# Optimization experiments

Hardware: AMD Instinct MI355X
Metric: run time of the kernel (lower is better)

The kernel has to match this reference:

```python
import jax, jax.numpy as jnp
import numpy as np

EPS = 1e-5
NEG_INF = float('-inf')

B, L, D = 4, 1024, 1024
H = 16
HD = D // H
I = 3280  # _round_to_multiple(3.2 * 1024, 8)
WIN = 256
STD = 0.01


def rmsnorm(x, w):
    x = jnp.clip(x.astype(jnp.float32), -10000.0, 10000.0)
    rms = jnp.sqrt(jnp.maximum(jnp.mean(x * x, axis=-1, keepdims=True), EPS) + EPS)
    out = x / rms * w
    return jnp.where(jnp.isfinite(out), out, jnp.zeros_like(out))


def setup_inputs() -> dict:
    key = jax.random.key(0)
    ks = jax.random.split(key, 12)
    inp = {
        'x': jax.random.normal(ks[0], (B, L, D), dtype=jnp.float32),
        'wq_w': jax.random.normal(ks[1], (D, D), dtype=jnp.float32) * STD,
        'wq_b': jnp.zeros((D,), jnp.float32),
        'wk_w': jax.random.normal(ks[2], (D, D), dtype=jnp.float32) * STD,
        'wk_b': jnp.zeros((D,), jnp.float32),
        'wv_w': jax.random.normal(ks[3], (D, D), dtype=jnp.float32) * STD,
        'wv_b': jnp.zeros((D,), jnp.float32),
        'wo_w': jax.random.normal(ks[4], (D, D), dtype=jnp.float32) * STD,
        'wo_b': jnp.zeros((D,), jnp.float32),
        'q_norm_w': jnp.ones((HD,), jnp.float32),
        'k_norm_w': jnp.ones((HD,), jnp.float32),
        'seq_norm_w': jnp.ones((D,), jnp.float32),
        'seq_post_norm_w': jnp.ones((D,), jnp.float32),
        'ffn_norm_w': jnp.ones((D,), jnp.float32),
        'ffn_post_norm_w': jnp.ones((D,), jnp.float32),
        'w1_w': jax.random.normal(ks[5], (I, D), dtype=jnp.float32) * STD,
        'w1_b': jnp.zeros((I,), jnp.float32),
        'w2_w': jax.random.normal(ks[6], (D, I), dtype=jnp.float32) * STD,
        'w2_b': jnp.zeros((D,), jnp.float32),
        'w3_w': jax.random.normal(ks[7], (I, D), dtype=jnp.float32) * STD,
        'w3_b': jnp.zeros((I,), jnp.float32),
        'window_size': WIN,
    }
    return inp


def attention(x, wq_w, wq_b, wk_w, wk_b, wv_w, wv_b, wo_w, wo_b, q_norm_w, k_norm_w, window_size):
    b, l, d = x.shape
    x = x.astype(jnp.float32)
    q = (x @ wq_w.T + wq_b).reshape(b, l, H, HD)
    k = (x @ wk_w.T + wk_b).reshape(b, l, H, HD)
    v = (x @ wv_w.T + wv_b).reshape(b, l, H, HD)
    q = rmsnorm(q, q_norm_w)
    k = rmsnorm(k, k_norm_w)
    scale = HD ** -0.5
    scores = jnp.einsum('blhd,bmhd->bhlm', q, k) * scale
    i = jnp.arange(l)[:, None]
    j = jnp.arange(l)[None, :]
    masked = (j > i) | (i - j >= window_size)  # True => forbidden
    scores = scores + jnp.where(masked, NEG_INF, 0.0)
    p = jax.nn.softmax(scores, axis=-1)
    attn = jnp.einsum('bhlm,bmhd->blhd', p, v)
    attn = jnp.where(jnp.isfinite(attn), attn, jnp.zeros_like(attn))
    attn = attn.reshape(b, l, d)
    return attn @ wo_w.T + wo_b


def swiglu(x, w1_w, w1_b, w2_w, w2_b, w3_w, w3_b):
    x = x.astype(jnp.float32)
    z1 = x @ w1_w.T + w1_b
    z3 = x @ w3_w.T + w3_b
    return (jax.nn.silu(z1) * z3) @ w2_w.T + w2_b


def reference(x, wq_w, wq_b, wk_w, wk_b, wv_w, wv_b, wo_w, wo_b,
              q_norm_w, k_norm_w, seq_norm_w, seq_post_norm_w,
              ffn_norm_w, ffn_post_norm_w,
              w1_w, w1_b, w2_w, w2_b, w3_w, w3_b, window_size):
    # seq_norm -> attn -> seq_post_norm -> residual
    a = attention(rmsnorm(x, seq_norm_w), wq_w, wq_b, wk_w, wk_b, wv_w, wv_b,
                  wo_w, wo_b, q_norm_w, k_norm_w, window_size)
    h = x + rmsnorm(a, seq_post_norm_w)
    # ffn_norm -> ffn -> ffn_post_norm -> residual
    f = swiglu(rmsnorm(h, ffn_norm_w), w1_w, w1_b, w2_w, w2_b, w3_w, w3_b)
    return h + rmsnorm(f, ffn_post_norm_w)
```

## Files before the change

kernel.cpp:

```cpp
#include <hip/hip_runtime.h>
#include <cmath>
#include <cstdint>

typedef __bf16 bf16;
typedef bf16 bf16x4 __attribute__((ext_vector_type(4)));
typedef bf16 bf16x8 __attribute__((ext_vector_type(8)));
typedef float f32x4 __attribute__((ext_vector_type(4)));
typedef unsigned int u32;
typedef u32 u32x4 __attribute__((ext_vector_type(4)));

#define EPS 1e-5f

__device__ __forceinline__ float clipf(float v) {
    return fminf(fmaxf(v, -10000.0f), 10000.0f);
}
__device__ __forceinline__ float fin0(float v) { return isfinite(v) ? v : 0.0f; }

__device__ __forceinline__ void async_copy16(void* lds, const void* g) {
    __builtin_amdgcn_global_load_lds((__attribute__((address_space(1))) void*)(void*)g,
                                     (__attribute__((address_space(3))) void*)lds,
                                     16, 0, 0);
}

__global__ __launch_bounds__(256) void prep(const float* __restrict__ wq, const float* __restrict__ wk,
                                            const float* __restrict__ wv, const float* __restrict__ wo,
                                            bf16* __restrict__ Wq, bf16* __restrict__ Wk,
                                            bf16* __restrict__ Wv, bf16* __restrict__ Wo,
                                            const float* __restrict__ w1, const float* __restrict__ w3,
                                            bf16* __restrict__ W1p, bf16* __restrict__ W3p,
                                            const float* __restrict__ w2, bf16* __restrict__ W2p,
                                            const float* __restrict__ x, const float* __restrict__ snw,
                                            bf16* __restrict__ xn) {
    const int bid = blockIdx.x, t = threadIdx.x;
    if (bid < 4096) {
        int z = bid >> 10, r = bid & 1023;
        const float* in = (z == 0) ? wq : (z == 1) ? wk : (z == 2) ? wv : wo;
        bf16* out = (z == 0) ? Wq : (z == 1) ? Wk : (z == 2) ? Wv : Wo;
        f32x4 v = ((const f32x4*)(in + (size_t)r * 1024))[t];
        bf16x4 o = {(bf16)v[0], (bf16)v[1], (bf16)v[2], (bf16)v[3]};
        ((bf16x4*)(out + (size_t)r * 1024))[t] = o;
    } else if (bid < 10752) {
        int b2 = bid - 4096;
        int which = b2 >= 3328;
        int r = b2 - (which ? 3328 : 0);
        const float* in = which ? w3 : w1;
        bf16* out = which ? W3p : W1p;
        bf16x4 o = {(bf16)0.f, (bf16)0.f, (bf16)0.f, (bf16)0.f};
        if (r < 3280) {
            f32x4 v = ((const f32x4*)(in + (size_t)r * 1024))[t];
            o[0] = (bf16)v[0]; o[1] = (bf16)v[1]; o[2] = (bf16)v[2]; o[3] = (bf16)v[3];
        }
        ((bf16x4*)(out + (size_t)r * 1024))[t] = o;
    } else if (bid < 11776) {
        int r = bid - 10752;
        for (int c4 = t * 4; c4 < 3328; c4 += 1024) {
            bf16x4 o = {(bf16)0.f, (bf16)0.f, (bf16)0.f, (bf16)0.f};
            if (c4 + 3 < 3280) {
                f32x4 v = *(const f32x4*)(w2 + (size_t)r * 3280 + c4);
                o[0] = (bf16)v[0]; o[1] = (bf16)v[1]; o[2] = (bf16)v[2]; o[3] = (bf16)v[3];
            } else {
                #pragma unroll
                for (int j = 0; j < 4; ++j)
                    if (c4 + j < 3280) o[j] = (bf16)w2[(size_t)r * 3280 + c4 + j];
            }
            *(bf16x4*)(W2p + (size_t)r * 3328 + c4) = o;
        }
    } else {
        __shared__ float sred[4];
        int row = bid - 11776;
        f32x4 xv = ((const f32x4*)(x + (size_t)row * 1024))[t];
        f32x4 cv;
        cv[0] = clipf(xv[0]); cv[1] = clipf(xv[1]); cv[2] = clipf(xv[2]); cv[3] = clipf(xv[3]);
        float ss = cv[0]*cv[0] + cv[1]*cv[1] + cv[2]*cv[2] + cv[3]*cv[3];
        #pragma unroll
        for (int off = 32; off >= 1; off >>= 1) ss += __shfl_xor(ss, off, 64);
        if ((t & 63) == 0) sred[t >> 6] = ss;
        __syncthreads();
        float tot = sred[0] + sred[1] + sred[2] + sred[3];
        float rms = sqrtf(fmaxf(tot * (1.0f / 1024.0f), EPS) + EPS);
        f32x4 wv_ = ((const f32x4*)snw)[t];
        bf16x4 o;
        o[0] = (bf16)fin0(cv[0] / rms * wv_[0]);
        o[1] = (bf16)fin0(cv[1] / rms * wv_[1]);
        o[2] = (bf16)fin0(cv[2] / rms * wv_[2]);
        o[3] = (bf16)fin0(cv[3] / rms * wv_[3]);
        *(bf16x4*)(xn + (size_t)row * 1024 + t * 4) = o;
    }
}

__global__ __launch_bounds__(512) void gemm_qkv3(const bf16* __restrict__ A,
                                                 const bf16* __restrict__ Bq,
                                                 const bf16* __restrict__ Bk,
                                                 const bf16* __restrict__ Bv,
                                                 const float* __restrict__ biq,
                                                 const float* __restrict__ bik,
                                                 const float* __restrict__ biv,
                                                 const float* __restrict__ qnw,
                                                 const float* __restrict__ knw,
                                                 bf16* __restrict__ Cq,
                                                 bf16* __restrict__ Ck,
                                                 bf16* __restrict__ VT) {
    __shared__ __align__(16) bf16 sA[2][128 * 32];
    __shared__ __align__(16) bf16 sBq[2][128 * 32];
    __shared__ __align__(16) bf16 sBk[2][128 * 32];
    __shared__ __align__(16) bf16 sBv[2][128 * 32];
    const int tid = threadIdx.x;
    const int w = tid >> 6, lane = tid & 63;
    const int m0 = blockIdx.x * 128;
    const int n0 = blockIdx.y * 128;
    const int mwo = (w >> 1) * 32;
    const int nwo = (w & 1) * 64;
    const int r16 = lane & 15, quad = lane >> 4;
    const int kreg = quad * 8;
    const int K = 1024, N = 1024;

    f32x4 zero = {0.f, 0.f, 0.f, 0.f};
    f32x4 aq[2][4], ak[2][4], av[2][4];
    #pragma unroll
    for (int i = 0; i < 2; ++i)
        #pragma unroll
        for (int j = 0; j < 4; ++j) { aq[i][j] = zero; ak[i][j] = zero; av[i][j] = zero; }

    const int arow = tid >> 2, akoff = (tid & 3) << 3;

    {
        async_copy16(&sA[0][tid * 8],  &A[(size_t)(m0 + arow) * K + akoff]);
        async_copy16(&sBq[0][tid * 8], &Bq[(size_t)(n0 + arow) * K + akoff]);
        async_copy16(&sBk[0][tid * 8], &Bk[(size_t)(n0 + arow) * K + akoff]);
        async_copy16(&sBv[0][tid * 8], &Bv[(size_t)(n0 + arow) * K + akoff]);
    }
    for (int kt = 0; kt < 32; ++kt) {
        __syncthreads();
        const int cur = kt & 1, nxt = cur ^ 1;
        if (kt + 1 < 32) {
            const int kb = (kt + 1) << 5;
            async_copy16(&sA[nxt][tid * 8],  &A[(size_t)(m0 + arow) * K + kb + akoff]);
            async_copy16(&sBq[nxt][tid * 8], &Bq[(size_t)(n0 + arow) * K + kb + akoff]);
            async_copy16(&sBk[nxt][tid * 8], &Bk[(size_t)(n0 + arow) * K + kb + akoff]);
            async_copy16(&sBv[nxt][tid * 8], &Bv[(size_t)(n0 + arow) * K + kb + akoff]);
        }
        bf16x8 af[2], bq_[4], bk_[4], bv_[4];
        #pragma unroll
        for (int i = 0; i < 2; ++i)
            af[i] = *(const bf16x8*)&sA[cur][(mwo + i * 16 + r16) * 32 + kreg];
        #pragma unroll
        for (int i = 0; i < 4; ++i) {
            bq_[i] = *(const bf16x8*)&sBq[cur][(nwo + i * 16 + r16) * 32 + kreg];
            bk_[i] = *(const bf16x8*)&sBk[cur][(nwo + i * 16 + r16) * 32 + kreg];
            bv_[i] = *(const bf16x8*)&sBv[cur][(nwo + i * 16 + r16) * 32 + kreg];
        }
        #pragma unroll
        for (int mi = 0; mi < 2; ++mi)
            #pragma unroll
            for (int ni = 0; ni < 4; ++ni) {
                aq[mi][ni] = __builtin_amdgcn_mfma_f32_16x16x32_bf16(af[mi], bq_[ni], aq[mi][ni], 0, 0, 0);
                ak[mi][ni] = __builtin_amdgcn_mfma_f32_16x16x32_bf16(af[mi], bk_[ni], ak[mi][ni], 0, 0, 0);
                av[mi][ni] = __builtin_amdgcn_mfma_f32_16x16x32_bf16(af[mi], bv_[ni], av[mi][ni], 0, 0, 0);
            }
    }

    float nwq[4], nwk[4], bvq[4], bvk[4], bvv[4];
    #pragma unroll
    for (int ni = 0; ni < 4; ++ni) {
        int col = n0 + nwo + ni * 16 + r16;
        bvq[ni] = biq[col]; bvk[ni] = bik[col]; bvv[ni] = biv[col];
        nwq[ni] = qnw[ni * 16 + r16]; nwk[ni] = knw[ni * 16 + r16];
    }
    #pragma unroll
    for (int s = 0; s < 2; ++s) {
        bf16* C = s ? Ck : Cq;
        #pragma unroll
        for (int mi = 0; mi < 2; ++mi) {
            #pragma unroll
            for (int r = 0; r < 4; ++r) {
                float v[4], ss = 0.0f;
                #pragma unroll
                for (int ni = 0; ni < 4; ++ni) {
                    float a = s ? ak[mi][ni][r] : aq[mi][ni][r];
                    v[ni] = clipf(a + (s ? bvk[ni] : bvq[ni]));
                    ss += v[ni] * v[ni];
                }
                ss += __shfl_xor(ss, 1, 64);
                ss += __shfl_xor(ss, 2, 64);
                ss += __shfl_xor(ss, 4, 64);
                ss += __shfl_xor(ss, 8, 64);
                float rms = sqrtf(fmaxf(ss * (1.0f / 64.0f), EPS) + EPS);
                int row = m0 + mwo + mi * 16 + quad * 4 + r;
                #pragma unroll
                for (int ni = 0; ni < 4; ++ni) {
                    int col = n0 + nwo + ni * 16 + r16;
                    float nw = s ? nwk[ni] : nwq[ni];
                    C[(size_t)row * N + col] = (bf16)fin0(v[ni] / rms * nw);
                }
            }
        }
    }
    {
        const int b_ = m0 >> 10;
        const int tokbase = (m0 & 1023) + mwo;
        #pragma unroll
        for (int ni = 0; ni < 4; ++ni) {
            int col = n0 + nwo + ni * 16 + r16;
            int h_ = col >> 6, hd = col & 63;
            bf16* dst = VT + (((size_t)b_ * 16 + h_) * 64 + hd) * 1024;
            #pragma unroll
            for (int mi = 0; mi < 2; ++mi) {
                bf16x4 pack;
                #pragma unroll
                for (int r = 0; r < 4; ++r) pack[r] = (bf16)(av[mi][ni][r] + bvv[ni]);
                *(bf16x4*)&dst[tokbase + mi * 16 + quad * 4] = pack;
            }
        }
    }
}

__global__ __launch_bounds__(512) void attn_win(const bf16* __restrict__ q,
                                                const bf16* __restrict__ k,
                                                const bf16* __restrict__ vt,
                                                const int* __restrict__ winp,
                                                bf16* __restrict__ o) {
    __shared__ __align__(16) bf16 sQ[128 * 64];
    __shared__ __align__(16) bf16 sK[64 * 64];
    __shared__ __align__(16) bf16 sVt[64 * 80];
    __shared__ __align__(16) bf16 sP[128 * 64];
    const int tid = threadIdx.x, w = tid >> 6, lane = tid & 63;
    const int qt = blockIdx.x, h = blockIdx.y, b = blockIdx.z;
    const int q0 = qt * 128;
    const int win = *winp;
    const float scale = 0.125f;
    const int r16 = lane & 15, quad = lane >> 4;

    {
        int c0 = tid, c1 = tid + 512;
        async_copy16(&sQ[c0 * 8], &q[(((size_t)b * 1024 + q0 + (c0 >> 3)) * 16 + h) * 64 + (c0 & 7) * 8]);
        async_copy16(&sQ[c1 * 8], &q[(((size_t)b * 1024 + q0 + (c1 >> 3)) * 16 + h) * 64 + (c1 & 7) * 8]);
    }
    __syncthreads();
    bf16x8 aq0 = *(const bf16x8*)&sQ[(w * 16 + r16) * 64 + quad * 8];
    bf16x8 aq1 = *(const bf16x8*)&sQ[(w * 16 + r16) * 64 + 32 + quad * 8];

    float Lr[4];
    f32x4 zero = {0.f, 0.f, 0.f, 0.f};
    f32x4 accO[4];
    #pragma unroll
    for (int r = 0; r < 4; ++r) Lr[r] = 0.0f;
    #pragma unroll
    for (int nf = 0; nf < 4; ++nf) accO[nf] = zero;

    int lo = q0 - (win - 1); if (lo < 0) lo = 0;
    const int kt0 = lo >> 6;
    const int ktend = (q0 + 127) >> 6;
    const bf16* vth = vt + ((size_t)b * 16 + h) * 64 * 1024;

    for (int kt = kt0; kt <= ktend; ++kt) {
        __syncthreads();
        async_copy16(&sK[tid * 8], &k[(((size_t)b * 1024 + kt * 64 + (tid >> 3)) * 16 + h) * 64 + (tid & 7) * 8]);
        {
            int hd = tid >> 3, koff = (tid & 7) * 8;
            *(u32x4*)&sVt[hd * 80 + koff] = *(const u32x4*)&vth[(size_t)hd * 1024 + kt * 64 + koff];
        }
        __syncthreads();

        f32x4 sf[4];
        #pragma unroll
        for (int nf = 0; nf < 4; ++nf) {
            bf16x8 bk0 = *(const bf16x8*)&sK[(nf * 16 + r16) * 64 + quad * 8];
            bf16x8 bk1 = *(const bf16x8*)&sK[(nf * 16 + r16) * 64 + 32 + quad * 8];
            f32x4 accS = zero;
            accS = __builtin_amdgcn_mfma_f32_16x16x32_bf16(aq0, bk0, accS, 0, 0, 0);
            accS = __builtin_amdgcn_mfma_f32_16x16x32_bf16(aq1, bk1, accS, 0, 0, 0);
            sf[nf] = accS;
        }

        #pragma unroll
        for (int r = 0; r < 4; ++r) {
            int i = q0 + w * 16 + quad * 4 + r;
            float ps = 0.0f;
            #pragma unroll
            for (int nf = 0; nf < 4; ++nf) {
                int j = kt * 64 + nf * 16 + r16;
                bool ok = (j <= i) && (i - j < win);
                float pv = ok ? __expf(sf[nf][r] * scale - 8.0f) : 0.0f;
                ps += pv;
                sP[(w * 16 + quad * 4 + r) * 64 + nf * 16 + r16] = (bf16)pv;
            }
            Lr[r] += ps;
        }
        __syncthreads();

        bf16x8 ap0 = *(const bf16x8*)&sP[(w * 16 + r16) * 64 + quad * 8];
        bf16x8 ap1 = *(const bf16x8*)&sP[(w * 16 + r16) * 64 + 32 + quad * 8];
        #pragma unroll
        for (int nf = 0; nf < 4; ++nf) {
            bf16x8 bv0 = *(const bf16x8*)&sVt[(nf * 16 + r16) * 80 + quad * 8];
            bf16x8 bv1 = *(const bf16x8*)&sVt[(nf * 16 + r16) * 80 + 32 + quad * 8];
            accO[nf] = __builtin_amdgcn_mfma_f32_16x16x32_bf16(ap0, bv0, accO[nf], 0, 0, 0);
            accO[nf] = __builtin_amdgcn_mfma_f32_16x16x32_bf16(ap1, bv1, accO[nf], 0, 0, 0);
        }
    }

    #pragma unroll
    for (int r = 0; r < 4; ++r) {
        float l = Lr[r];
        l += __shfl_xor(l, 1, 64);
        l += __shfl_xor(l, 2, 64);
        l += __shfl_xor(l, 4, 64);
        l += __shfl_xor(l, 8, 64);
        float inv = (l > 0.0f) ? 1.0f / l : 0.0f;
        int row = q0 + w * 16 + quad * 4 + r;
        #pragma unroll
        for (int nf = 0; nf < 4; ++nf) {
            float ov = fin0(accO[nf][r] * inv);
            o[(((size_t)b * 1024 + row) * 16 + h) * 64 + nf * 16 + r16] = (bf16)ov;
        }
    }
}

__global__ __launch_bounds__(512) void gemm_sk2(const bf16* __restrict__ A,
                                                const bf16* __restrict__ B,
                                                float* __restrict__ P,
                                                int K, int Kh) {
    __shared__ __align__(16) bf16 sA[2][256 * 32];
    __shared__ __align__(16) bf16 sB[2][128 * 32];
    const int tid = threadIdx.x;
    const int w = tid >> 6, lane = tid & 63;
    const int m0 = blockIdx.x * 256, n0 = blockIdx.y * 128;
    const int mwo = (w & 3) * 64, nwo = (w >> 2) * 64;
    const int r16 = lane & 15, quad = lane >> 4, kreg = quad * 8;
    const int kbase = blockIdx.z * Kh;
    const int N = 1024;

    const int ar0 = tid >> 2,        ak0 = (tid & 3) << 3;
    const int c1 = tid + 512;
    const int ar1 = c1 >> 2,         ak1 = (c1 & 3) << 3;
    const int br = tid >> 2,         bk = (tid & 3) << 3;

    f32x4 zero = {0.f, 0.f, 0.f, 0.f};
    f32x4 acc[4][4];
    #pragma unroll
    for (int i = 0; i < 4; ++i)
        #pragma unroll
        for (int j = 0; j < 4; ++j) acc[i][j] = zero;

    {
        async_copy16(&sA[0][tid * 8], &A[(size_t)(m0 + ar0) * K + kbase + ak0]);
        async_copy16(&sA[0][c1 * 8],  &A[(size_t)(m0 + ar1) * K + kbase + ak1]);
        async_copy16(&sB[0][tid * 8], &B[(size_t)(n0 + br) * K + kbase + bk]);
    }
    const int kIters = Kh >> 5;
    for (int kt = 0; kt < kIters; ++kt) {
        __syncthreads();
        const int cur = kt & 1, nxt = cur ^ 1;
        if (kt + 1 < kIters) {
            const int kb = kbase + ((kt + 1) << 5);
            async_copy16(&sA[nxt][tid * 8], &A[(size_t)(m0 + ar0) * K + kb + ak0]);
            async_copy16(&sA[nxt][c1 * 8],  &A[(size_t)(m0 + ar1) * K + kb + ak1]);
            async_copy16(&sB[nxt][tid * 8], &B[(size_t)(n0 + br) * K + kb + bk]);
        }
        bf16x8 af[4], bfr[4];
        #pragma unroll
        for (int i = 0; i < 4; ++i) {
            af[i]  = *(const bf16x8*)&sA[cur][(mwo + i * 16 + r16) * 32 + kreg];
            bfr[i] = *(const bf16x8*)&sB[cur][(nwo + i * 16 + r16) * 32 + kreg];
        }
        #pragma unroll
        for (int mi = 0; mi < 4; ++mi)
            #pragma unroll
            for (int ni = 0; ni < 4; ++ni)
                acc[mi][ni] = __builtin_amdgcn_mfma_f32_16x16x32_bf16(af[mi], bfr[ni], acc[mi][ni], 0, 0, 0);
    }

    float* Pz = P + (size_t)blockIdx.z * 4096 * 1024;
    #pragma unroll
    for (int mi = 0; mi < 4; ++mi)
        #pragma unroll
        for (int ni = 0; ni < 4; ++ni) {
            int col = n0 + nwo + ni * 16 + r16;
            #pragma unroll
            for (int r = 0; r < 4; ++r) {
                int row = m0 + mwo + mi * 16 + quad * 4 + r;
                Pz[(size_t)row * N + col] = acc[mi][ni][r];
            }
        }
}

template <bool EMIT>
__global__ __launch_bounds__(512) void resid_norm(const float* __restrict__ xres,
                                                  const float* __restrict__ p0,
                                                  const float* __restrict__ p1,
                                                  const float* __restrict__ bias,
                                                  const float* __restrict__ wpost,
                                                  const float* __restrict__ wnext,
                                                  float* __restrict__ hout,
                                                  bf16* __restrict__ hnout) {
    __shared__ float sred[8];
    const int tid = threadIdx.x;
    const int grp = tid >> 8, t = tid & 255;
    const int w4 = (tid >> 6) & 3;
    for (int it = 0; it < 4; ++it) {
        int row = it * 1024 + blockIdx.x * 2 + grp;
        f32x4 a0 = ((const f32x4*)(p0 + (size_t)row * 1024))[t];
        f32x4 a1 = ((const f32x4*)(p1 + (size_t)row * 1024))[t];
        f32x4 bv = ((const f32x4*)bias)[t];
        f32x4 af;
        af[0] = clipf(a0[0] + a1[0] + bv[0]);
        af[1] = clipf(a0[1] + a1[1] + bv[1]);
        af[2] = clipf(a0[2] + a1[2] + bv[2]);
        af[3] = clipf(a0[3] + a1[3] + bv[3]);
        float ss = af[0]*af[0] + af[1]*af[1] + af[2]*af[2] + af[3]*af[3];
        #pragma unroll
        for (int off = 32; off >= 1; off >>= 1) ss += __shfl_xor(ss, off, 64);
        __syncthreads();
        if ((tid & 63) == 0) sred[grp * 4 + w4] = ss;
        __syncthreads();
        float tot = sred[grp*4+0] + sred[grp*4+1] + sred[grp*4+2] + sred[grp*4+3];
        float rms1 = sqrtf(fmaxf(tot * (1.0f / 1024.0f), EPS) + EPS);
        f32x4 xv = ((const f32x4*)(xres + (size_t)row * 1024))[t];
        f32x4 wp = ((const f32x4*)wpost)[t];
        f32x4 hv;
        hv[0] = xv[0] + fin0(af[0] / rms1 * wp[0]);
        hv[1] = xv[1] + fin0(af[1] / rms1 * wp[1]);
        hv[2] = xv[2] + fin0(af[2] / rms1 * wp[2]);
        hv[3] = xv[3] + fin0(af[3] / rms1 * wp[3]);
        ((f32x4*)(hout + (size_t)row * 1024))[t] = hv;
        if (EMIT) {
            f32x4 cv;
            cv[0] = clipf(hv[0]); cv[1] = clipf(hv[1]); cv[2] = clipf(hv[2]); cv[3] = clipf(hv[3]);
            float ss2 = cv[0]*cv[0] + cv[1]*cv[1] + cv[2]*cv[2] + cv[3]*cv[3];
            #pragma unroll
            for (int off = 32; off >= 1; off >>= 1) ss2 += __shfl_xor(ss2, off, 64);
            __syncthreads();
            if ((tid & 63) == 0) sred[grp * 4 + w4] = ss2;
            __syncthreads();
            float tot2 = sred[grp*4+0] + sred[grp*4+1] + sred[grp*4+2] + sred[grp*4+3];
            float rms2 = sqrtf(fmaxf(tot2 * (1.0f / 1024.0f), EPS) + EPS);
            f32x4 wn = ((const f32x4*)wnext)[t];
            bf16x4 o;
            o[0] = (bf16)fin0(cv[0] / rms2 * wn[0]);
            o[1] = (bf16)fin0(cv[1] / rms2 * wn[1]);
            o[2] = (bf16)fin0(cv[2] / rms2 * wn[2]);
            o[3] = (bf16)fin0(cv[3] / rms2 * wn[3]);
            *(bf16x4*)(hnout + (size_t)row * 1024 + t * 4) = o;
        }
    }
}

__global__ __launch_bounds__(512) void gemm_ffn1(const bf16* __restrict__ A,
                                                 const bf16* __restrict__ B1,
                                                 const bf16* __restrict__ B3,
                                                 const float* __restrict__ b1,
                                                 const float* __restrict__ b3,
                                                 bf16* __restrict__ G) {
    __shared__ __align__(16) bf16 sA[2][128 * 32];
    __shared__ __align__(16) bf16 sB1[2][128 * 32];
    __shared__ __align__(16) bf16 sB3[2][128 * 32];
    const int tid = threadIdx.x;
    const int w = tid >> 6, lane = tid & 63;
    const int m0 = blockIdx.x * 128;
    const int n0 = blockIdx.y * 128;
    const int mwo = (w >> 2) * 64, nwo = (w & 3) * 32;
    const int r16 = lane & 15, quad = lane >> 4;
    const int kreg = quad * 8;
    const int K = 1024, N = 3328;

    f32x4 zero = {0.f, 0.f, 0.f, 0.f};
    f32x4 acc1[4][2], acc3[4][2];
    #pragma unroll
    for (int i = 0; i < 4; ++i)
        #pragma unroll
        for (int j = 0; j < 2; ++j) { acc1[i][j] = zero; acc3[i][j] = zero; }

    const int arow = tid >> 2, akoff = (tid & 3) << 3;

    {
        async_copy16(&sA[0][tid * 8],  &A[(size_t)(m0 + arow) * K + akoff]);
        async_copy16(&sB1[0][tid * 8], &B1[(size_t)(n0 + arow) * K + akoff]);
        async_copy16(&sB3[0][tid * 8], &B3[(size_t)(n0 + arow) * K + akoff]);
    }
    for (int kt = 0; kt < 32; ++kt) {
        __syncthreads();
        const int cur = kt & 1, nxt = cur ^ 1;
        if (kt + 1 < 32) {
            const int kb = (kt + 1) << 5;
            async_copy16(&sA[nxt][tid * 8],  &A[(size_t)(m0 + arow) * K + kb + akoff]);
            async_copy16(&sB1[nxt][tid * 8], &B1[(size_t)(n0 + arow) * K + kb + akoff]);
            async_copy16(&sB3[nxt][tid * 8], &B3[(size_t)(n0 + arow) * K + kb + akoff]);
        }
        bf16x8 af[4], bf1[2], bf3[2];
        #pragma unroll
        for (int i = 0; i < 4; ++i)
            af[i]  = *(const bf16x8*)&sA[cur][(mwo + i * 16 + r16) * 32 + kreg];
        #pragma unroll
        for (int i = 0; i < 2; ++i) {
            bf1[i] = *(const bf16x8*)&sB1[cur][(nwo + i * 16 + r16) * 32 + kreg];
            bf3[i] = *(const bf16x8*)&sB3[cur][(nwo + i * 16 + r16) * 32 + kreg];
        }
        #pragma unroll
        for (int mi = 0; mi < 4; ++mi)
            #pragma unroll
            for (int ni = 0; ni < 2; ++ni) {
                acc1[mi][ni] = __builtin_amdgcn_mfma_f32_16x16x32_bf16(af[mi], bf1[ni], acc1[mi][ni], 0, 0, 0);
                acc3[mi][ni] = __builtin_amdgcn_mfma_f32_16x16x32_bf16(af[mi], bf3[ni], acc3[mi][ni], 0, 0, 0);
            }
    }

    #pragma unroll
    for (int ni = 0; ni < 2; ++ni) {
        int col = n0 + nwo + ni * 16 + r16;
        float bv1 = (col < 3280) ? b1[col] : 0.0f;
        float bv3 = (col < 3280) ? b3[col] : 0.0f;
        #pragma unroll
        for (int mi = 0; mi < 4; ++mi) {
            #pragma unroll
            for (int r = 0; r < 4; ++r) {
                int row = m0 + mwo + mi * 16 + quad * 4 + r;
                float z1 = acc1[mi][ni][r] + bv1;
                float z3 = acc3[mi][ni][r] + bv3;
                float s = z1 / (1.0f + __expf(-z1));
                G[(size_t)row * N + col] = (bf16)(s * z3);
            }
        }
    }
}

extern "C" void kernel_launch(void* const* d_in, const int* in_sizes, int n_in,
                              void* d_out, int out_size, void* d_ws, size_t ws_size,
                              hipStream_t stream) {
    const float* x       = (const float*)d_in[0];
    const float* wq_w    = (const float*)d_in[1];
    const float* wq_b    = (const float*)d_in[2];
    const float* wk_w    = (const float*)d_in[3];
    const float* wk_b    = (const float*)d_in[4];
    const float* wv_w    = (const float*)d_in[5];
    const float* wv_b    = (const float*)d_in[6];
    const float* wo_w    = (const float*)d_in[7];
    const float* wo_b    = (const float*)d_in[8];
    const float* q_norm_w= (const float*)d_in[9];
    const float* k_norm_w= (const float*)d_in[10];
    const float* seq_norm_w      = (const float*)d_in[11];
    const float* seq_post_norm_w = (const float*)d_in[12];
    const float* ffn_norm_w      = (const float*)d_in[13];
    const float* ffn_post_norm_w = (const float*)d_in[14];
    const float* w1_w    = (const float*)d_in[15];
    const float* w1_b    = (const float*)d_in[16];
    const float* w2_w    = (const float*)d_in[17];
    const float* w2_b    = (const float*)d_in[18];
    const float* w3_w    = (const float*)d_in[19];
    const float* w3_b    = (const float*)d_in[20];
    const int*   winp    = (const int*)d_in[21];
    float* out = (float*)d_out;

    const size_t SZ_W   = 2097152;
    const size_t SZ_WP  = 6815744;
    const size_t SZ_ACT = 8388608;
    const size_t SZ_H   = 16777216;
    const size_t SZ_P   = 33554432;

    char* p = (char*)d_ws;
    bf16* Wq  = (bf16*)p; p += SZ_W;
    bf16* Wk  = (bf16*)p; p += SZ_W;
    bf16* Wv  = (bf16*)p; p += SZ_W;
    bf16* Wo  = (bf16*)p; p += SZ_W;
    bf16* W1p = (bf16*)p; p += SZ_WP;
    bf16* W3p = (bf16*)p; p += SZ_WP;
    bf16* W2p = (bf16*)p; p += SZ_WP;
    float* h  = (float*)p; p += SZ_H;
    bf16* hn  = (bf16*)p; p += SZ_ACT;
    float* part = (float*)p; p += SZ_P;
    float* part1 = part + (size_t)4096 * 1024;
    char* regionA = p;
    bf16* xn    = (bf16*)(regionA);
    bf16* qb    = (bf16*)(regionA + 1 * SZ_ACT);
    bf16* kb    = (bf16*)(regionA + 2 * SZ_ACT);
    bf16* vtb   = (bf16*)(regionA + 3 * SZ_ACT);
    bf16* attnb = (bf16*)(regionA + 4 * SZ_ACT);
    bf16* g     = (bf16*)(regionA);

    prep<<<dim3(15872), dim3(256), 0, stream>>>(wq_w, wk_w, wv_w, wo_w, Wq, Wk, Wv, Wo,
                                                w1_w, w3_w, W1p, W3p, w2_w, W2p,
                                                x, seq_norm_w, xn);

    gemm_qkv3<<<dim3(32, 8), dim3(512), 0, stream>>>(xn, Wq, Wk, Wv, wq_b, wk_b, wv_b,
                                                     q_norm_w, k_norm_w, qb, kb, vtb);

    attn_win<<<dim3(8, 16, 4), dim3(512), 0, stream>>>(qb, kb, vtb, winp, attnb);

    gemm_sk2<<<dim3(16, 8, 2), dim3(512), 0, stream>>>(attnb, Wo, part, 1024, 512);

    resid_norm<true><<<dim3(512), dim3(512), 0, stream>>>(x, part, part1, wo_b,
                                                          seq_post_norm_w, ffn_norm_w, h, hn);

    gemm_ffn1<<<dim3(32, 26), dim3(512), 0, stream>>>(hn, W1p, W3p, w1_b, w3_b, g);

    gemm_sk2<<<dim3(16, 8, 2), dim3(512), 0, stream>>>(g, W2p, part, 3328, 1664);

    resid_norm<false><<<dim3(512), dim3(512), 0, stream>>>(h, part, part1, w2_b,
                                                           ffn_post_norm_w, nullptr, out, nullptr);
}
```

Before: 381.9 us.

## Overlap Wo/FFN weight conversion with QKV GEMM by merging into its grid

Moves the fp32-to-bf16 conversion of Wo, W1, W3 and W2 out of the prep kernel and into extra blocks appended to the QKV GEMM grid, which is flattened to 1D. Those conversion blocks run alongside the 256 GEMM tiles and fill CUs the GEMM leaves idle, taking the conversion off the critical path. The conversion blocks share the GEMM's 512-thread launch and large LDS allocation, which may limit how many of them fit per CU, and their memory traffic now competes with the GEMM's.

```diff
diff --git a/kernel.cpp b/kernel.cpp
--- a/kernel.cpp
+++ b/kernel.cpp
@@ -23,51 +23,22 @@
 }
 
 __global__ __launch_bounds__(256) void prep(const float* __restrict__ wq, const float* __restrict__ wk,
-                                            const float* __restrict__ wv, const float* __restrict__ wo,
+                                            const float* __restrict__ wv,
                                             bf16* __restrict__ Wq, bf16* __restrict__ Wk,
-                                            bf16* __restrict__ Wv, bf16* __restrict__ Wo,
-                                            const float* __restrict__ w1, const float* __restrict__ w3,
-                                            bf16* __restrict__ W1p, bf16* __restrict__ W3p,
-                                            const float* __restrict__ w2, bf16* __restrict__ W2p,
+                                            bf16* __restrict__ Wv,
                                             const float* __restrict__ x, const float* __restrict__ snw,
                                             bf16* __restrict__ xn) {
     const int bid = blockIdx.x, t = threadIdx.x;
-    if (bid < 4096) {
+    if (bid < 3072) {
         int z = bid >> 10, r = bid & 1023;
-        const float* in = (z == 0) ? wq : (z == 1) ? wk : (z == 2) ? wv : wo;
-        bf16* out = (z == 0) ? Wq : (z == 1) ? Wk : (z == 2) ? Wv : Wo;
+        const float* in = (z == 0) ? wq : (z == 1) ? wk : wv;
+        bf16* out = (z == 0) ? Wq : (z == 1) ? Wk : Wv;
         f32x4 v = ((const f32x4*)(in + (size_t)r * 1024))[t];
         bf16x4 o = {(bf16)v[0], (bf16)v[1], (bf16)v[2], (bf16)v[3]};
         ((bf16x4*)(out + (size_t)r * 1024))[t] = o;
-    } else if (bid < 10752) {
-        int b2 = bid - 4096;
-        int which = b2 >= 3328;
-        int r = b2 - (which ? 3328 : 0);
-        const float* in = which ? w3 : w1;
-        bf16* out = which ? W3p : W1p;
-        bf16x4 o = {(bf16)0.f, (bf16)0.f, (bf16)0.f, (bf16)0.f};
-        if (r < 3280) {
-            f32x4 v = ((const f32x4*)(in + (size_t)r * 1024))[t];
-            o[0] = (bf16)v[0]; o[1] = (bf16)v[1]; o[2] = (bf16)v[2]; o[3] = (bf16)v[3];
-        }
-        ((bf16x4*)(out + (size_t)r * 1024))[t] = o;
-    } else if (bid < 11776) {
-        int r = bid - 10752;
-        for (int c4 = t * 4; c4 < 3328; c4 += 1024) {
-            bf16x4 o = {(bf16)0.f, (bf16)0.f, (bf16)0.f, (bf16)0.f};
-            if (c4 + 3 < 3280) {
-                f32x4 v = *(const f32x4*)(w2 + (size_t)r * 3280 + c4);
-                o[0] = (bf16)v[0]; o[1] = (bf16)v[1]; o[2] = (bf16)v[2]; o[3] = (bf16)v[3];
-            } else {
-                #pragma unroll
-                for (int j = 0; j < 4; ++j)
-                    if (c4 + j < 3280) o[j] = (bf16)w2[(size_t)r * 3280 + c4 + j];
-            }
-            *(bf16x4*)(W2p + (size_t)r * 3328 + c4) = o;
-        }
     } else {
         __shared__ float sred[4];
-        int row = bid - 11776;
+        int row = bid - 3072;
         f32x4 xv = ((const f32x4*)(x + (size_t)row * 1024))[t];
         f32x4 cv;
         cv[0] = clipf(xv[0]); cv[1] = clipf(xv[1]); cv[2] = clipf(xv[2]); cv[3] = clipf(xv[3]);
@@ -99,15 +70,62 @@
                                                  const float* __restrict__ knw,
                                                  bf16* __restrict__ Cq,
                                                  bf16* __restrict__ Ck,
-                                                 bf16* __restrict__ VT) {
+                                                 bf16* __restrict__ VT,
+                                                 const float* __restrict__ wo,
+                                                 const float* __restrict__ w1,
+                                                 const float* __restrict__ w3,
+                                                 const float* __restrict__ w2,
+                                                 bf16* __restrict__ Wo,
+                                                 bf16* __restrict__ W1p,
+                                                 bf16* __restrict__ W3p,
+                                                 bf16* __restrict__ W2p) {
     __shared__ __align__(16) bf16 sA[2][128 * 32];
     __shared__ __align__(16) bf16 sBq[2][128 * 32];
     __shared__ __align__(16) bf16 sBk[2][128 * 32];
     __shared__ __align__(16) bf16 sBv[2][128 * 32];
     const int tid = threadIdx.x;
+
+    if (blockIdx.x >= 256) {
+        const int cid = blockIdx.x - 256;
+        const int grp = tid >> 8;
+        const int t = tid & 255;
+        const int u = cid * 2 + grp;
+        if (u < 1024) {
+            f32x4 v = ((const f32x4*)(wo + (size_t)u * 1024))[t];
+            bf16x4 o = {(bf16)v[0], (bf16)v[1], (bf16)v[2], (bf16)v[3]};
+            ((bf16x4*)(Wo + (size_t)u * 1024))[t] = o;
+        } else if (u < 7680) {
+            int which = u >= 4352;
+            int r = u - (which ? 4352 : 1024);
+            const float* in = which ? w3 : w1;
+            bf16* out = which ? W3p : W1p;
+            bf16x4 o = {(bf16)0.f, (bf16)0.f, (bf16)0.f, (bf16)0.f};
+            if (r < 3280) {
+                f32x4 v = ((const f32x4*)(in + (size_t)r * 1024))[t];
+                o[0] = (bf16)v[0]; o[1] = (bf16)v[1]; o[2] = (bf16)v[2]; o[3] = (bf16)v[3];
+            }
+            ((bf16x4*)(out + (size_t)r * 1024))[t] = o;
+        } else {
+            int r = u - 7680;
+            for (int c4 = t * 4; c4 < 3328; c4 += 1024) {
+                bf16x4 o = {(bf16)0.f, (bf16)0.f, (bf16)0.f, (bf16)0.f};
+                if (c4 + 3 < 3280) {
+                    f32x4 v = *(const f32x4*)(w2 + (size_t)r * 3280 + c4);
+                    o[0] = (bf16)v[0]; o[1] = (bf16)v[1]; o[2] = (bf16)v[2]; o[3] = (bf16)v[3];
+                } else {
+                    #pragma unroll
+                    for (int j = 0; j < 4; ++j)
+                        if (c4 + j < 3280) o[j] = (bf16)w2[(size_t)r * 3280 + c4 + j];
+                }
+                *(bf16x4*)(W2p + (size_t)r * 3328 + c4) = o;
+            }
+        }
+        return;
+    }
+
     const int w = tid >> 6, lane = tid & 63;
-    const int m0 = blockIdx.x * 128;
-    const int n0 = blockIdx.y * 128;
+    const int m0 = (blockIdx.x & 31) * 128;
+    const int n0 = (blockIdx.x >> 5) * 128;
     const int mwo = (w >> 1) * 32;
     const int nwo = (w & 1) * 64;
     const int r16 = lane & 15, quad = lane >> 4;
@@ -576,12 +594,13 @@
     bf16* attnb = (bf16*)(regionA + 4 * SZ_ACT);
     bf16* g     = (bf16*)(regionA);
 
-    prep<<<dim3(15872), dim3(256), 0, stream>>>(wq_w, wk_w, wv_w, wo_w, Wq, Wk, Wv, Wo,
-                                                w1_w, w3_w, W1p, W3p, w2_w, W2p,
-                                                x, seq_norm_w, xn);
-
-    gemm_qkv3<<<dim3(32, 8), dim3(512), 0, stream>>>(xn, Wq, Wk, Wv, wq_b, wk_b, wv_b,
-                                                     q_norm_w, k_norm_w, qb, kb, vtb);
+    prep<<<dim3(7168), dim3(256), 0, stream>>>(wq_w, wk_w, wv_w, Wq, Wk, Wv,
+                                               x, seq_norm_w, xn);
+
+    gemm_qkv3<<<dim3(4608), dim3(512), 0, stream>>>(xn, Wq, Wk, Wv, wq_b, wk_b, wv_b,
+                                                    q_norm_w, k_norm_w, qb, kb, vtb,
+                                                    wo_w, w1_w, w3_w, w2_w,
+                                                    Wo, W1p, W3p, W2p);
 
     attn_win<<<dim3(8, 16, 4), dim3(512), 0, stream>>>(qb, kb, vtb, winp, attnb);
 
```

Measured after the change: 389.5 us. 1.02x slower.
